# Optimization experiments

Hardware: AMD Instinct MI355X
Metric: run time of the kernel (lower is better)

## Reference

```python
import jax, jax.numpy as jnp
import numpy as np

N_NODES = 10000
N_EDGES = 640000
D_IN = 128
D_OUT = 128


def setup_inputs() -> dict:
    key = jax.random.key(0)
    k1, k2, k3, k4 = jax.random.split(key, 4)
    x = jax.random.normal(k1, (N_NODES, D_IN), dtype=jnp.float32)
    # PyG GCNConv weight: [dim_out, dim_in] (glorot)
    W = jax.random.normal(k2, (D_OUT, D_IN), dtype=jnp.float32) * (1.0 / np.sqrt(D_IN))
    b = jnp.zeros((D_OUT,), dtype=jnp.float32)
    edge_weight = jax.random.uniform(k3, (N_EDGES,), dtype=jnp.float32)
    edge_index = jax.random.randint(k4, (2, N_EDGES), 0, N_NODES, dtype=jnp.int32)
    return {"x": x, "W": W, "b": b, "edge_weight": edge_weight, "edge_index": edge_index}


def reference(x, W, b, edge_weight, edge_index):
    N = x.shape[0]
    # --- add self loops (fill weight = 1.0), PyG default ---
    loops = jnp.arange(N, dtype=edge_index.dtype)
    src = jnp.concatenate([edge_index[0], loops])
    dst = jnp.concatenate([edge_index[1], loops])
    ew = jnp.concatenate([edge_weight, jnp.ones((N,), dtype=edge_weight.dtype)])
    # --- symmetric GCN normalization: deg from target index ---
    deg = jax.ops.segment_sum(ew, dst, num_segments=N)
    dinv = jnp.where(deg > 0, jax.lax.rsqrt(deg), 0.0)
    norm = dinv[src] * ew * dinv[dst]  # [E+N]
    # --- linear transform then gather-scale-scatter aggregation ---
    h = x @ W.T  # [N, D_OUT]
    msgs = h[src] * norm[:, None]  # [E+N, D_OUT]
    out = jax.ops.segment_sum(msgs, dst, num_segments=N)
    return out + b
```

## Files before the change

kernel.cpp:

```cpp
#include <hip/hip_runtime.h>

#define N_NODES 10000
#define N_EDGES 640000
#define D 128
#define CAP 128

typedef unsigned long long ull;
typedef unsigned short u16;
typedef unsigned int u32;

#define CHUNKS 128
#define EPC 5000
#define NR 250
#define RW 40
#define CELLCAP 64
#define GEMM_NPB 32
#define GEMM_BLOCKS ((N_NODES + GEMM_NPB - 1) / GEMM_NPB)
#define SMEM_A 16384
#define SMEM_CSR (CHUNKS * CELLCAP * 8)
#define EWFX 262144.0f
#define EWM  0x1ffffffu

__device__ __forceinline__ u16 f2bf(float f) {
    unsigned u = __float_as_uint(f);
    unsigned r = (u + 0x7fffu + ((u >> 16) & 1u)) >> 16;
    return (u16)r;
}


__global__ void __launch_bounds__(256) k_bucket(
    const int* __restrict__ src, const int* __restrict__ dst,
    const float* __restrict__ ew, const float* __restrict__ x,
    const float* __restrict__ W, u16* __restrict__ h_bf,
    u32* __restrict__ counts, ull* __restrict__ ebuf)
{
    extern __shared__ char smem[];
    const int t = threadIdx.x;

    if (blockIdx.x < CHUNKS) {
        u32* rcnt = (u32*)smem;
        if (t < NR) rcnt[t] = 0;
        __syncthreads();

        const int e0 = blockIdx.x * EPC;
        #pragma unroll
        for (int i = 0; i < 20; ++i) {
            int idx = i * 256 + t;
            if (idx < EPC) {
                int e = e0 + idx;
                int d = dst[e];
                int s = src[e];
                float w = ew[e];
                int r = d / RW;
                int bin = d - r * RW;
                u32 slot = atomicAdd(&rcnt[r], 1u);
                if (slot < CELLCAP) {
                    ull rec = ((ull)__float_as_uint(w) << 32)
                            | ((u32)s << 6) | (u32)bin;
                    ebuf[((size_t)r * CHUNKS + blockIdx.x) * CELLCAP + slot] = rec;
                }
            }
        }
        __syncthreads();

        if (t < NR) counts[blockIdx.x * NR + t] = rcnt[t];
    } else {
        float* xs = (float*)smem;
        const int node0 = (blockIdx.x - CHUNKS) * GEMM_NPB;
        const int col = t & 127;
        const int half = t >> 7;

        #pragma unroll
        for (int r = 0; r < 16; ++r) {
            int row = half * 16 + r;
            int n = node0 + row;
            xs[row * D + col] = (n < N_NODES) ? x[n * D + col] : 0.0f;
        }
        __syncthreads();

        float acc[16];
        #pragma unroll
        for (int r = 0; r < 16; ++r) acc[r] = 0.0f;

        const float4* Wrow = (const float4*)&W[col * D];
        const float* xbase = &xs[half * 16 * D];
        for (int k4 = 0; k4 < D / 4; ++k4) {
            float4 w = Wrow[k4];
            int k = k4 * 4;
            #pragma unroll
            for (int r = 0; r < 16; ++r) {
                acc[r] += xbase[r * D + k + 0] * w.x;
                acc[r] += xbase[r * D + k + 1] * w.y;
                acc[r] += xbase[r * D + k + 2] * w.z;
                acc[r] += xbase[r * D + k + 3] * w.w;
            }
        }
        #pragma unroll
        for (int r = 0; r < 16; ++r) {
            int n = node0 + half * 16 + r;
            if (n < N_NODES) h_bf[n * D + col] = f2bf(acc[r]);
        }
    }
}


__global__ void __launch_bounds__(512) k_csr(
    const u32* __restrict__ counts, const ull* __restrict__ ebuf,
    u32* __restrict__ gpacked, float* __restrict__ dinv, ull* __restrict__ csr)
{
    extern __shared__ char smem[];
    ull* sbuf = (ull*)smem;
    __shared__ u32 bcnt[RW];
    __shared__ u32 ccnt[CHUNKS];
    const int t = threadIdx.x;
    const int r = blockIdx.x;

    {
        const uint4* colg = (const uint4*)(ebuf + (size_t)r * CHUNKS * CELLCAP);
        uint4* cols = (uint4*)sbuf;
        #pragma unroll
        for (int i = 0; i < (CHUNKS * CELLCAP / 2) / 512; ++i)
            cols[i * 512 + t] = colg[i * 512 + t];
    }
    if (t < RW) bcnt[t] = 0;
    if (t < CHUNKS) {
        u32 c = counts[t * NR + r];
        ccnt[t] = (c > CELLCAP) ? (u32)CELLCAP : c;
    }
    __syncthreads();

    {
        const int g = t >> 2;
        const int l = t & 3;
        const int cnt = (int)ccnt[g];
        const ull* cell = sbuf + g * CELLCAP;
        for (int s = l; s < cnt; s += 4) {
            ull rec = cell[s];
            u32 lo = (u32)rec;
            int bin = (int)(lo & 63u);
            u32 srcn = lo >> 6;
            u32 wbits = (u32)(rec >> 32);
            float w = __uint_as_float(wbits);
            u32 add = (1u << 25) | (u32)(w * EWFX);
            u32 old = atomicAdd(&bcnt[bin], add);
            int pos = (int)(old >> 25);
            if (pos < CAP) {
                int dstg = r * RW + bin;
                csr[(size_t)dstg * CAP + pos] = ((ull)wbits << 32) | srcn;
            }
        }
    }
    __syncthreads();

    if (t < RW) {
        int n = r * RW + t;
        u32 v = bcnt[t];
        gpacked[n] = v;
        dinv[n] = rsqrtf(1.0f + (float)(v & EWM) * 0x1p-18f);
    }
}


#define AGG_NPB 4

__global__ void __launch_bounds__(256) k_agg(
    const u32* __restrict__ gpacked, const float* __restrict__ dinv,
    const ull* __restrict__ csr, const u16* __restrict__ h_bf,
    const float* __restrict__ b, float* __restrict__ out)
{
    const int wid  = threadIdx.x >> 6;
    const int lane = threadIdx.x & 63;
    const int n = blockIdx.x * AGG_NPB + wid;

    __shared__ ull sm[AGG_NPB][CAP];

    const int deg = (int)(gpacked[n] >> 25);
    const float dn = dinv[n];
    const ull* bucket = csr + (size_t)n * CAP;

    #pragma unroll
    for (int r = 0; r < 2; ++r) {
        int j = r * 64 + lane;
        if (j < deg) {
            ull v = bucket[j];
            int s = (int)(u32)(v & 0xffffffffu);
            float w = __uint_as_float((u32)(v >> 32));
            float nm = dinv[s] * w * dn;
            sm[wid][j] = ((ull)__float_as_uint(nm) << 32) | (u32)s;
        }
    }
    __syncthreads();

    float acc0 = 0.0f, acc1 = 0.0f;
    const ull* smw = sm[wid];
    #pragma unroll 4
    for (int j = 0; j < deg; ++j) {
        ull v = smw[j];
        int s = (int)(u32)v;
        float nm = __uint_as_float((u32)(v >> 32));
        u32 hc = *(const u32*)(h_bf + (size_t)s * D + lane * 2);
        acc0 += __uint_as_float(hc << 16) * nm;
        acc1 += __uint_as_float(hc & 0xffff0000u) * nm;
    }

    float s2 = dn * dn;
    u32 hs = *(const u32*)(h_bf + (size_t)n * D + lane * 2);
    acc0 += __uint_as_float(hs << 16) * s2;
    acc1 += __uint_as_float(hs & 0xffff0000u) * s2;
    float2 bb = *(const float2*)(b + lane * 2);
    float2 o;
    o.x = acc0 + bb.x;
    o.y = acc1 + bb.y;
    *(float2*)(out + (size_t)n * D + lane * 2) = o;
}


extern "C" void kernel_launch(void* const* d_in, const int* in_sizes, int n_in,
                              void* d_out, int out_size, void* d_ws, size_t ws_size,
                              hipStream_t stream) {
    const float* x  = (const float*)d_in[0];
    const float* W  = (const float*)d_in[1];
    const float* b  = (const float*)d_in[2];
    const float* ew = (const float*)d_in[3];
    const int* ei   = (const int*)d_in[4];
    const int* src = ei;
    const int* dst = ei + N_EDGES;
    float* out = (float*)d_out;

    char* ws = (char*)d_ws;
    u32*   gpacked = (u32*)(ws);
    float* dinv    = (float*)(ws + 40000);
    u16*   h_bf    = (u16*)(ws + 80000);
    ull*   csr     = (ull*)(ws + 2640000);
    u32*   counts  = (u32*)(ws + 12880000);
    ull*   ebuf    = (ull*)(ws + 13008000);

    k_bucket<<<CHUNKS + GEMM_BLOCKS, 256, SMEM_A, stream>>>(
        src, dst, ew, x, W, h_bf, counts, ebuf);
    k_csr<<<NR, 512, SMEM_CSR, stream>>>(counts, ebuf, gpacked, dinv, csr);
    k_agg<<<N_NODES / AGG_NPB, 256, 0, stream>>>(gpacked, dinv, csr, h_bf, b, out);
}
```

Before: 115.0 us.

## Use finer edge buckets with in-band sentinels and register-resident CSR build

```diff
diff --git a/kernel.cpp b/kernel.cpp
--- a/kernel.cpp
+++ b/kernel.cpp
@@ -9,15 +9,14 @@
 typedef unsigned short u16;
 typedef unsigned int u32;
 
-#define CHUNKS 128
-#define EPC 5000
-#define NR 250
-#define RW 40
-#define CELLCAP 64
+#define CHUNKS 512
+#define EPC 1250
+#define NR 500
+#define RW 20
+#define CELLCAP 20
 #define GEMM_NPB 32
 #define GEMM_BLOCKS ((N_NODES + GEMM_NPB - 1) / GEMM_NPB)
-#define SMEM_A 16384
-#define SMEM_CSR (CHUNKS * CELLCAP * 8)
+#define SMEM_K1 16384
 #define EWFX 262144.0f
 #define EWM  0x1ffffffu
 
@@ -32,19 +31,19 @@
     const int* __restrict__ src, const int* __restrict__ dst,
     const float* __restrict__ ew, const float* __restrict__ x,
     const float* __restrict__ W, u16* __restrict__ h_bf,
-    u32* __restrict__ counts, ull* __restrict__ ebuf)
+    ull* __restrict__ ebuf)
 {
     extern __shared__ char smem[];
     const int t = threadIdx.x;
 
     if (blockIdx.x < CHUNKS) {
         u32* rcnt = (u32*)smem;
-        if (t < NR) rcnt[t] = 0;
+        for (int i = t; i < NR; i += 256) rcnt[i] = 0;
         __syncthreads();
 
         const int e0 = blockIdx.x * EPC;
         #pragma unroll
-        for (int i = 0; i < 20; ++i) {
+        for (int i = 0; i < 5; ++i) {
             int idx = i * 256 + t;
             if (idx < EPC) {
                 int e = e0 + idx;
@@ -55,15 +54,18 @@
                 int bin = d - r * RW;
                 u32 slot = atomicAdd(&rcnt[r], 1u);
                 if (slot < CELLCAP) {
-                    ull rec = ((ull)__float_as_uint(w) << 32)
-                            | ((u32)s << 6) | (u32)bin;
-                    ebuf[((size_t)r * CHUNKS + blockIdx.x) * CELLCAP + slot] = rec;
+                    ebuf[((size_t)r * CHUNKS + blockIdx.x) * CELLCAP + slot] =
+                        ((ull)__float_as_uint(w) << 32) | ((u32)s << 5) | (u32)bin;
                 }
             }
         }
         __syncthreads();
 
-        if (t < NR) counts[blockIdx.x * NR + t] = rcnt[t];
+        for (int i = t; i < NR; i += 256) {
+            u32 slot = rcnt[i];
+            if (slot < CELLCAP)
+                ebuf[((size_t)i * CHUNKS + blockIdx.x) * CELLCAP + slot] = 31ull;
+        }
     } else {
         float* xs = (float*)smem;
         const int node0 = (blockIdx.x - CHUNKS) * GEMM_NPB;
@@ -104,49 +106,45 @@
 }
 
 
+#define REC(s) (((s) & 1) ? (((ull)rr[(s) >> 1].w << 32) | (ull)rr[(s) >> 1].z) \
+                          : (((ull)rr[(s) >> 1].y << 32) | (ull)rr[(s) >> 1].x))
+
 __global__ void __launch_bounds__(512) k_csr(
-    const u32* __restrict__ counts, const ull* __restrict__ ebuf,
-    u32* __restrict__ gpacked, float* __restrict__ dinv, ull* __restrict__ csr)
+    const ull* __restrict__ ebuf, u32* __restrict__ gpacked,
+    float* __restrict__ dinv, ull* __restrict__ csr)
 {
-    extern __shared__ char smem[];
-    ull* sbuf = (ull*)smem;
     __shared__ u32 bcnt[RW];
-    __shared__ u32 ccnt[CHUNKS];
     const int t = threadIdx.x;
     const int r = blockIdx.x;
 
-    {
-        const uint4* colg = (const uint4*)(ebuf + (size_t)r * CHUNKS * CELLCAP);
-        uint4* cols = (uint4*)sbuf;
-        #pragma unroll
-        for (int i = 0; i < (CHUNKS * CELLCAP / 2) / 512; ++i)
-            cols[i * 512 + t] = colg[i * 512 + t];
-    }
     if (t < RW) bcnt[t] = 0;
-    if (t < CHUNKS) {
-        u32 c = counts[t * NR + r];
-        ccnt[t] = (c > CELLCAP) ? (u32)CELLCAP : c;
-    }
+
+    uint4 rr[CELLCAP / 2];
+    const uint4* pb = (const uint4*)(ebuf + ((size_t)r * CHUNKS + t) * CELLCAP);
+    #pragma unroll
+    for (int i = 0; i < CELLCAP / 2; ++i) rr[i] = pb[i];
     __syncthreads();
 
-    {
-        const int g = t >> 2;
-        const int l = t & 3;
-        const int cnt = (int)ccnt[g];
-        const ull* cell = sbuf + g * CELLCAP;
-        for (int s = l; s < cnt; s += 4) {
-            ull rec = cell[s];
-            u32 lo = (u32)rec;
-            int bin = (int)(lo & 63u);
-            u32 srcn = lo >> 6;
-            u32 wbits = (u32)(rec >> 32);
-            float w = __uint_as_float(wbits);
+    int cnt = CELLCAP;
+    #pragma unroll
+    for (int s = CELLCAP - 1; s >= 0; --s)
+        if (((u32)REC(s) & 31u) == 31u) cnt = s;
+
+    #pragma unroll
+    for (int s = 0; s < CELLCAP; ++s) {
+        if (s < cnt) {
+            ull v = REC(s);
+            u32 lo = (u32)v;
+            int bin = (int)(lo & 31u);
+            u32 srcn = lo >> 5;
+            u32 wb = (u32)(v >> 32);
+            float w = __uint_as_float(wb);
             u32 add = (1u << 25) | (u32)(w * EWFX);
             u32 old = atomicAdd(&bcnt[bin], add);
             int pos = (int)(old >> 25);
             if (pos < CAP) {
                 int dstg = r * RW + bin;
-                csr[(size_t)dstg * CAP + pos] = ((ull)wbits << 32) | srcn;
+                csr[(size_t)dstg * CAP + pos] = ((ull)wb << 32) | srcn;
             }
         }
     }
@@ -232,11 +230,10 @@
     float* dinv    = (float*)(ws + 40000);
     u16*   h_bf    = (u16*)(ws + 80000);
     ull*   csr     = (ull*)(ws + 2640000);
-    u32*   counts  = (u32*)(ws + 12880000);
-    ull*   ebuf    = (ull*)(ws + 13008000);
-
-    k_bucket<<<CHUNKS + GEMM_BLOCKS, 256, SMEM_A, stream>>>(
-        src, dst, ew, x, W, h_bf, counts, ebuf);
-    k_csr<<<NR, 512, SMEM_CSR, stream>>>(counts, ebuf, gpacked, dinv, csr);
+    ull*   ebuf    = (ull*)(ws + 12880000);
+
+    k_bucket<<<CHUNKS + GEMM_BLOCKS, 256, SMEM_K1, stream>>>(
+        src, dst, ew, x, W, h_bf, ebuf);
+    k_csr<<<NR, 512, 0, stream>>>(ebuf, gpacked, dinv, csr);
     k_agg<<<N_NODES / AGG_NPB, 256, 0, stream>>>(gpacked, dinv, csr, h_bf, b, out);
 }
```

Measured after the change: 121.8 us. 1.06x slower.
